# Kernel optimization log

Hardware: AMD Instinct MI355X
Metric: run time of the kernel (lower is better)

The kernel has to match this reference:

```python
import jax, jax.numpy as jnp
import numpy as np

B, S, H0G, H1G, H0E, H1E, A, E = 16384, 512, 512, 256, 1024, 512, 64, 4


def setup_inputs() -> dict:
    key = jax.random.key(0)
    ks = jax.random.split(key, 8)
    rn = lambda k, shape, s=0.05: jax.random.normal(k, shape, jnp.float32) * s
    return {
        "x": rn(ks[0], (B, S), 1.0),
        # Gating network params (Normalizer + 2 tanh layers + fca, softmax outside)
        "g_mean": jnp.zeros((S,), jnp.float32),
        "g_std": jnp.ones((S,), jnp.float32),
        "gW0": rn(ks[1], (S, H0G)), "gb0": jnp.zeros((H0G,), jnp.float32),
        "gW1": rn(ks[2], (H0G, H1G)), "gb1": jnp.zeros((H1G,), jnp.float32),
        "gWa": rn(ks[3], (H1G, E)), "gba": jnp.zeros((E,), jnp.float32),
        # 4 expert Actors, weights stacked along leading expert axis E
        "e_mean": jnp.zeros((E, S), jnp.float32),
        "e_std": jnp.ones((E, S), jnp.float32),
        "eW0": rn(ks[4], (E, S, H0E)), "eb0": jnp.zeros((E, H0E), jnp.float32),
        "eW1": rn(ks[5], (E, H0E, H1E)), "eb1": jnp.zeros((E, H1E), jnp.float32),
        "eWa": rn(ks[6], (E, H1E, A), 0.001), "eba": jnp.zeros((E, A), jnp.float32),
        "scale": jnp.ones((A,), jnp.float32),  # (a_max - a_min) / 2
    }


def reference(x, g_mean, g_std, gW0, gb0, gW1, gb1, gWa, gba,
              e_mean, e_std, eW0, eb0, eW1, eb1, eWa, eba, scale):
    # Gating: normalize -> tanh MLP -> linear -> softmax over experts
    xg = (x - g_mean) / g_std                                   # [B,S]
    h = jnp.tanh(xg @ gW0 + gb0)
    h = jnp.tanh(h @ gW1 + gb1)
    w = jax.nn.softmax(h @ gWa + gba, axis=-1)                  # [B,E]

    # Experts (Actor.forward), batched over expert axis e
    xe = (x[None, :, :] - e_mean[:, None, :]) / e_std[:, None, :]          # [E,B,S]
    he = jnp.tanh(jnp.einsum('ebs,esh->ebh', xe, eW0) + eb0[:, None, :])   # [E,B,H0E]
    he = jnp.tanh(jnp.einsum('ebh,ehk->ebk', he, eW1) + eb1[:, None, :])   # [E,B,H1E]
    a = (jnp.einsum('ebk,eka->eba', he, eWa) + eba[:, None, :]) * scale    # [E,B,A]

    # Weighted combination of expert action means
    return jnp.einsum('be,eba->ba', w, a)                       # [B,A]
```

## Files before the change

### kernel.cpp

```cpp
#include <hip/hip_runtime.h>
#include <hip/hip_bf16.h>

typedef _Float16 f16;
typedef _Float16 f16x4 __attribute__((ext_vector_type(4)));
typedef _Float16 f16x8 __attribute__((ext_vector_type(8)));
typedef float f32x4 __attribute__((ext_vector_type(4)));

#define DEV static __device__ __forceinline__

DEV void gld_lds16(const void* g, void* l) {
  __builtin_amdgcn_global_load_lds(
      (const __attribute__((address_space(1))) void*)g,
      (__attribute__((address_space(3))) void*)l, 16, 0, 0);
}

DEV float fast_tanh(float x) {
  float e = __expf(2.0f * x);
  return 1.0f - 2.0f / (e + 1.0f);
}

DEV int xcd_swizzle(int raw, int nwg) {
  return ((nwg & 7) == 0) ? ((raw & 7) * (nwg >> 3) + (raw >> 3)) : raw;
}

__global__ __launch_bounds__(256) void k_cvt_x(const float* __restrict__ x,
                                               f16* __restrict__ xh, long n) {
  long i0 = ((long)blockIdx.x * 256 + threadIdx.x) * 4;
  long stride = (long)gridDim.x * 1024;
  for (long i = i0; i < n; i += stride) {
    const float4 v = *(const float4*)(x + i);
    f16x4 h;
    h.x = (f16)v.x; h.y = (f16)v.y; h.z = (f16)v.z; h.w = (f16)v.w;
    *(f16x4*)(xh + i) = h;
  }
}

__global__ __launch_bounds__(256) void k_transpose(const float* __restrict__ in,
                                                   f16* __restrict__ out,
                                                   const float* __restrict__ stdv,
                                                   int K_, int N_) {
  __shared__ float tile[32][33];
  const int e = blockIdx.z;
  const float* ine = in + (long)e * K_ * N_;
  f16* oute = out + (long)e * K_ * N_;
  const int n0 = blockIdx.x * 32, k0 = blockIdx.y * 32;
  const int tx = threadIdx.x, ty = threadIdx.y;
#pragma unroll
  for (int j = 0; j < 4; j++)
    tile[ty + j * 8][tx] = ine[(long)(k0 + ty + j * 8) * N_ + n0 + tx];
  __syncthreads();
  const float rs = stdv ? 1.0f / stdv[(long)e * K_ + k0 + tx] : 1.0f;
#pragma unroll
  for (int j = 0; j < 4; j++)
    oute[(long)(n0 + ty + j * 8) * K_ + k0 + tx] = (f16)(tile[tx][ty + j * 8] * rs);
}

__global__ __launch_bounds__(1024) void k_bias_corr(const float* __restrict__ W,
                                                    const float* __restrict__ b,
                                                    const float* __restrict__ mean,
                                                    const float* __restrict__ stdv,
                                                    float* __restrict__ outb,
                                                    int S_, int H_) {
  __shared__ float red[16][64];
  const int e = blockIdx.y;
  const float* We = W + (long)e * S_ * H_;
  const float* me = mean + (long)e * S_;
  const float* se = stdv + (long)e * S_;
  const int h = blockIdx.x * 64 + threadIdx.x;
  const int sl = threadIdx.y;
  float acc = 0.0f;
#pragma unroll 4
  for (int s = sl; s < S_; s += 16) acc += (me[s] / se[s]) * We[(long)s * H_ + h];
  red[sl][threadIdx.x] = acc;
  __syncthreads();
  if (sl == 0) {
    float a = 0.0f;
#pragma unroll
    for (int j = 0; j < 16; j++) a += red[j][threadIdx.x];
    outb[(long)e * H_ + h] = b[(long)e * H_ + h] - a;
  }
}

__global__ __launch_bounds__(256) void k_gemm_cv(
    const f16* __restrict__ A, const f16* __restrict__ Bt,
    const float* __restrict__ bias, f16* __restrict__ C,
    int M, int K, int lda, int ldb, int ldc,
    long sA, long sB, long sBias, long sC) {
  A += (long)blockIdx.z * sA; Bt += (long)blockIdx.z * sB;
  bias += (long)blockIdx.z * sBias; C += (long)blockIdx.z * sC;
  extern __shared__ __align__(16) f16 lds[];
  const int tid = threadIdx.x, wave = tid >> 6, lane = tid & 63;
  const int nwg = gridDim.x * gridDim.y;
  const int logical = xcd_swizzle(blockIdx.y * gridDim.x + blockIdx.x, nwg);
  const int bx = logical % gridDim.x, by = logical / gridDim.x;
  const int m0 = by * 128, n0 = bx * 128;
  const int wr = wave >> 1, wc = wave & 1;
  f32x4 acc[4][4] = {};
  const int swz = (tid & 7) ^ ((tid >> 3) & 7);
  const f16* Ag = A + (long)(m0 + (tid >> 3)) * lda + swz * 8;
  const f16* Bg = Bt + (long)(n0 + (tid >> 3)) * ldb + swz * 8;
  const int wo = wave * 512;

#define STG_A(bufi, tile)                                         \
  { f16* _d = lds + (bufi) * 8192 + wo;                           \
    const long _k = (long)(tile) << 6;                            \
    gld_lds16(Ag + _k, _d);                                       \
    gld_lds16(Ag + (long)32 * lda + _k, _d + 2048);               \
    gld_lds16(Ag + (long)64 * lda + _k, _d + 4096);               \
    gld_lds16(Ag + (long)96 * lda + _k, _d + 6144); }
#define STG_B(bufi, tile)                                         \
  { f16* _d = lds + 24576 + (bufi) * 8192 + wo;                   \
    const long _k = (long)(tile) << 6;                            \
    gld_lds16(Bg + _k, _d);                                       \
    gld_lds16(Bg + (long)32 * ldb + _k, _d + 2048);               \
    gld_lds16(Bg + (long)64 * ldb + _k, _d + 4096);               \
    gld_lds16(Bg + (long)96 * ldb + _k, _d + 6144); }

  const int nt = K >> 6;
  STG_A(0, 0)
  STG_B(0, 0)
  STG_A(1, 1)
  asm volatile("s_waitcnt vmcnt(4)" ::: "memory");
  __builtin_amdgcn_s_barrier();
  asm volatile("" ::: "memory");

  for (int t = 0; t < nt; ++t) {
    if (t + 1 < nt) STG_B((t + 1) & 1, t + 1)
    if (t + 2 < nt) STG_A((t + 2) % 3, t + 2)
    const f16* Abuf = lds + (t % 3) * 8192;
    const f16* Bbuf = lds + 24576 + (t & 1) * 8192;
#pragma unroll
    for (int kk = 0; kk < 2; kk++) {
      f16x8 af[4], bfr[4];
      const int rchunk = (kk * 4 + (lane >> 4)) ^ (lane & 7);
#pragma unroll
      for (int mi = 0; mi < 4; mi++)
        af[mi] = *(const f16x8*)&Abuf[(wr * 64 + mi * 16 + (lane & 15)) * 64 + rchunk * 8];
#pragma unroll
      for (int ni = 0; ni < 4; ni++)
        bfr[ni] = *(const f16x8*)&Bbuf[(wc * 64 + ni * 16 + (lane & 15)) * 64 + rchunk * 8];
#pragma unroll
      for (int mi = 0; mi < 4; mi++)
#pragma unroll
        for (int ni = 0; ni < 4; ni++)
          acc[mi][ni] = __builtin_amdgcn_mfma_f32_16x16x32_f16(af[mi], bfr[ni], acc[mi][ni], 0, 0, 0);
    }
    if (t + 2 < nt) {
      asm volatile("s_waitcnt vmcnt(4)" ::: "memory");
    } else {
      asm volatile("s_waitcnt vmcnt(0)" ::: "memory");
    }
    __builtin_amdgcn_s_barrier();
    asm volatile("" ::: "memory");
  }
#undef STG_A
#undef STG_B

  const int r0 = (lane >> 4) * 4, cb = lane & 15;
#pragma unroll
  for (int ni = 0; ni < 4; ni++) {
    const int col = n0 + wc * 64 + ni * 16 + cb;
    const float bc = bias[col];
#pragma unroll
    for (int mi = 0; mi < 4; mi++) {
      const int row = m0 + wr * 64 + mi * 16 + r0;
#pragma unroll
      for (int r = 0; r < 4; r++)
        C[(long)(row + r) * ldc + col] = (f16)fast_tanh(acc[mi][ni][r] + bc);
    }
  }
}

__global__ __launch_bounds__(256) void k_gating_head(const f16* __restrict__ h1,
                                                     const float* __restrict__ gWa,
                                                     const float* __restrict__ gba,
                                                     float* __restrict__ gw, int B_) {
  const int b = blockIdx.x * 4 + (threadIdx.x >> 6);
  const int lane = threadIdx.x & 63;
  const f16x4 hv = *(const f16x4*)&h1[(long)b * 256 + lane * 4];
  float s0 = 0, s1 = 0, s2 = 0, s3 = 0;
#pragma unroll
  for (int j = 0; j < 4; j++) {
    const float hh = (float)hv[j];
    const float4 wr4 = *(const float4*)&gWa[(lane * 4 + j) * 4];
    s0 += hh * wr4.x; s1 += hh * wr4.y; s2 += hh * wr4.z; s3 += hh * wr4.w;
  }
#pragma unroll
  for (int off = 32; off >= 1; off >>= 1) {
    s0 += __shfl_xor(s0, off);
    s1 += __shfl_xor(s1, off);
    s2 += __shfl_xor(s2, off);
    s3 += __shfl_xor(s3, off);
  }
  const float l0 = s0 + gba[0], l1 = s1 + gba[1], l2 = s2 + gba[2], l3 = s3 + gba[3];
  float mx = fmaxf(fmaxf(l0, l1), fmaxf(l2, l3));
  const float e0 = __expf(l0 - mx), e1 = __expf(l1 - mx), e2 = __expf(l2 - mx), e3 = __expf(l3 - mx);
  const float inv = 1.0f / (e0 + e1 + e2 + e3);
  if (lane == 0) {
    float4 o; o.x = e0 * inv; o.y = e1 * inv; o.z = e2 * inv; o.w = e3 * inv;
    *(float4*)&gw[(long)b * 4] = o;
  }
}

__global__ __launch_bounds__(256) void k_head2(const f16* __restrict__ he1,
                                               const f16* __restrict__ Wt,
                                               const float* __restrict__ eba,
                                               const float* __restrict__ scale,
                                               const float* __restrict__ gw,
                                               float* __restrict__ out,
                                               long sA) {
  constexpr int K = 512;
  __shared__ __align__(16) f16 As[2][64 * 64];
  __shared__ __align__(16) f16 Bs[2][64 * 64];
  const int tid = threadIdx.x, wave = tid >> 6, lane = tid & 63;
  const int bid = xcd_swizzle(blockIdx.x, gridDim.x);
  const long m0 = (long)bid * 64;
  const int swz = (tid & 7) ^ ((tid >> 3) & 7);
  const f16* Ag = he1 + (m0 + tid / 8) * K + swz * 8;
  const f16* Bg = Wt + (long)(tid / 8) * K + swz * 8;
  const int wo = wave * 512;
  const int r0 = (lane >> 4) * 4, cb = lane & 15;
  float4 gwv[4];
#pragma unroll
  for (int r = 0; r < 4; r++)
    gwv[r] = *(const float4*)&gw[(m0 + wave * 16 + r0 + r) * 4];
  f32x4 osum[4] = {};
  f32x4 acc[4] = {};

#pragma unroll
  for (int i = 0; i < 2; i++) {
    gld_lds16(Ag + (long)i * 32 * K, &As[0][wo + i * 2048]);
    gld_lds16(Bg + (long)i * 32 * K, &Bs[0][wo + i * 2048]);
  }
  __syncthreads();
  int cur = 0;
#pragma unroll
  for (int e = 0; e < 4; e++) {
    for (int kt = 0; kt < 8; ++kt) {
      const int s = e * 8 + kt;
      if (s + 1 < 32) {
        const int sn = s + 1;
        const long ae = (long)(sn >> 3) * sA + ((sn & 7) << 6);
        const long be = (long)(sn >> 3) * (64 * K) + ((sn & 7) << 6);
#pragma unroll
        for (int i = 0; i < 2; i++) {
          gld_lds16(Ag + ae + (long)i * 32 * K, &As[cur ^ 1][wo + i * 2048]);
          gld_lds16(Bg + be + (long)i * 32 * K, &Bs[cur ^ 1][wo + i * 2048]);
        }
      }
#pragma unroll
      for (int kk = 0; kk < 2; kk++) {
        const int rchunk = (kk * 4 + (lane >> 4)) ^ (lane & 7);
        const f16x8 a = *(const f16x8*)&As[cur][(wave * 16 + (lane & 15)) * 64 + rchunk * 8];
#pragma unroll
        for (int ni = 0; ni < 4; ni++) {
          const f16x8 bq = *(const f16x8*)&Bs[cur][(ni * 16 + (lane & 15)) * 64 + rchunk * 8];
          acc[ni] = __builtin_amdgcn_mfma_f32_16x16x32_f16(a, bq, acc[ni], 0, 0, 0);
        }
      }
      __syncthreads();
      cur ^= 1;
    }
#pragma unroll
    for (int ni = 0; ni < 4; ni++)
#pragma unroll
      for (int r = 0; r < 4; r++) {
        const float ge = (e == 0) ? gwv[r].x : (e == 1) ? gwv[r].y
                        : (e == 2) ? gwv[r].z : gwv[r].w;
        osum[ni][r] += ge * acc[ni][r];
        acc[ni][r] = 0.0f;
      }
  }

#pragma unroll
  for (int ni = 0; ni < 4; ni++) {
    const int col = ni * 16 + cb;
    const float sc = scale[col];
#pragma unroll
    for (int r = 0; r < 4; r++) {
      const long row = m0 + wave * 16 + r0 + r;
      const float b4 = gwv[r].x * eba[col] + gwv[r].y * eba[64 + col] +
                       gwv[r].z * eba[128 + col] + gwv[r].w * eba[192 + col];
      out[row * 64 + col] = (osum[ni][r] + b4) * sc;
    }
  }
}

__global__ __launch_bounds__(256) void k_head(const f16* __restrict__ he1,
                                              const f16* __restrict__ Wt,
                                              const float* __restrict__ ebae,
                                              const float* __restrict__ scale,
                                              const float* __restrict__ gw,
                                              float* __restrict__ outa,
                                              int e0, int K,
                                              long sA, long sB, long sBias, long sC) {
  const int z = blockIdx.z;
  he1 += (long)z * sA; Wt += (long)z * sB; ebae += (long)z * sBias; outa += (long)z * sC;
  const int e = e0 + z;
  __shared__ __align__(16) f16 As[2][64 * 64];
  __shared__ __align__(16) f16 Bs[2][64 * 64];
  const int tid = threadIdx.x, wave = tid >> 6, lane = tid & 63;
  const int bid = xcd_swizzle(blockIdx.x, gridDim.x);
  const long m0 = (long)bid * 64;
  f32x4 acc[4] = {};
  const int swz = (tid & 7) ^ ((tid >> 3) & 7);
  const f16* Ag = he1 + (m0 + tid / 8) * K + swz * 8;
  const f16* Bg = Wt + (long)(tid / 8) * K + swz * 8;
  const int wo = wave * 512;
#pragma unroll
  for (int i = 0; i < 2; i++) {
    gld_lds16(Ag + (long)i * 32 * K, &As[0][wo + i * 2048]);
    gld_lds16(Bg + (long)i * 32 * K, &Bs[0][wo + i * 2048]);
  }
  __syncthreads();
  const int nt = K >> 6;
  int cur = 0;
  for (int t = 0; t < nt; ++t) {
    if (t + 1 < nt) {
      const long kt = (long)(t + 1) << 6;
#pragma unroll
      for (int i = 0; i < 2; i++) {
        gld_lds16(Ag + (long)i * 32 * K + kt, &As[cur ^ 1][wo + i * 2048]);
        gld_lds16(Bg + (long)i * 32 * K + kt, &Bs[cur ^ 1][wo + i * 2048]);
      }
    }
#pragma unroll
    for (int kk = 0; kk < 2; kk++) {
      const int rchunk = (kk * 4 + (lane >> 4)) ^ (lane & 7);
      const f16x8 a = *(const f16x8*)&As[cur][(wave * 16 + (lane & 15)) * 64 + rchunk * 8];
#pragma unroll
      for (int ni = 0; ni < 4; ni++) {
        const f16x8 bq = *(const f16x8*)&Bs[cur][(ni * 16 + (lane & 15)) * 64 + rchunk * 8];
        acc[ni] = __builtin_amdgcn_mfma_f32_16x16x32_f16(a, bq, acc[ni], 0, 0, 0);
      }
    }
    __syncthreads();
    cur ^= 1;
  }
  const int r0 = (lane >> 4) * 4, cb = lane & 15;
#pragma unroll
  for (int ni = 0; ni < 4; ni++) {
    const int col = ni * 16 + cb;
    const float sb = scale[col], bb = ebae[col];
    const long row0 = m0 + wave * 16 + r0;
#pragma unroll
    for (int r = 0; r < 4; r++) {
      const long row = row0 + r;
      outa[row * 64 + col] = (acc[ni][r] + bb) * sb * gw[row * 4 + e];
    }
  }
}

__global__ __launch_bounds__(256) void k_combine(const float* __restrict__ a_all,
                                                 float* __restrict__ out, long n) {
  long i = ((long)blockIdx.x * 256 + threadIdx.x) * 4;
  if (i < n) {
    const float4 v0 = *(const float4*)(a_all + i);
    const float4 v1 = *(const float4*)(a_all + n + i);
    const float4 v2 = *(const float4*)(a_all + 2 * n + i);
    const float4 v3 = *(const float4*)(a_all + 3 * n + i);
    float4 o;
    o.x = v0.x + v1.x + v2.x + v3.x;
    o.y = v0.y + v1.y + v2.y + v3.y;
    o.z = v0.z + v1.z + v2.z + v3.z;
    o.w = v0.w + v1.w + v2.w + v3.w;
    *(float4*)(out + i) = o;
  }
}

extern "C" void kernel_launch(void* const* d_in, const int* in_sizes, int n_in,
                              void* d_out, int out_size, void* d_ws, size_t ws_size,
                              hipStream_t stream) {
  constexpr int Bn = 16384, S = 512, H0G = 512, H1G = 256, H0E = 1024, H1E = 512, A = 64, E = 4;
  const float* x      = (const float*)d_in[0];
  const float* g_mean = (const float*)d_in[1];
  const float* g_std  = (const float*)d_in[2];
  const float* gW0    = (const float*)d_in[3];
  const float* gb0    = (const float*)d_in[4];
  const float* gW1    = (const float*)d_in[5];
  const float* gb1    = (const float*)d_in[6];
  const float* gWa    = (const float*)d_in[7];
  const float* gba    = (const float*)d_in[8];
  const float* e_mean = (const float*)d_in[9];
  const float* e_std  = (const float*)d_in[10];
  const float* eW0    = (const float*)d_in[11];
  const float* eb0    = (const float*)d_in[12];
  const float* eW1    = (const float*)d_in[13];
  const float* eb1    = (const float*)d_in[14];
  const float* eWa    = (const float*)d_in[15];
  const float* eba    = (const float*)d_in[16];
  const float* scale  = (const float*)d_in[17];
  float* out = (float*)d_out;

  char* p = (char*)d_ws;
  auto alloc = [&](size_t bytes) { char* q = p; p += (bytes + 255) & ~(size_t)255; return q; };
  f16* xh    = (f16*)alloc((size_t)Bn * S * 2);
  float* gw  = (float*)alloc((size_t)Bn * E * 4);
  float* a_all = (float*)alloc((size_t)E * Bn * A * 4);
  f16* gW0t  = (f16*)alloc((size_t)S * H0G * 2);
  f16* gW1t  = (f16*)alloc((size_t)H0G * H1G * 2);
  f16* eW0t  = (f16*)alloc((size_t)E * S * H0E * 2);
  f16* eW1t  = (f16*)alloc((size_t)E * H0E * H1E * 2);
  f16* eWat  = (f16*)alloc((size_t)E * H1E * A * 2);
  float* gb0c = (float*)alloc((size_t)H0G * 4);
  float* eb0c = (float*)alloc((size_t)E * H0E * 4);
  f16* h0g   = (f16*)alloc((size_t)Bn * H0G * 2);
  const size_t base = (size_t)(p - (char*)d_ws);
  const size_t per_g = ((size_t)Bn * H0E * 2 + 256) + ((size_t)Bn * H1E * 2 + 256);
  int g = 1;
  if (ws_size >= base + 4 * per_g) g = 4;
  else if (ws_size >= base + 2 * per_g) g = 2;
  f16* he0_g = (f16*)alloc((size_t)g * Bn * H0E * 2);
  f16* he1_g = (f16*)alloc((size_t)g * Bn * H1E * 2);
  f16* h1g = he1_g;

  k_cvt_x<<<2048, 256, 0, stream>>>(x, xh, (long)Bn * S);
  k_transpose<<<dim3(H0G / 32, S / 32, 1), dim3(32, 8), 0, stream>>>(gW0, gW0t, g_std, S, H0G);
  k_transpose<<<dim3(H1G / 32, H0G / 32, 1), dim3(32, 8), 0, stream>>>(gW1, gW1t, nullptr, H0G, H1G);
  k_transpose<<<dim3(H0E / 32, S / 32, E), dim3(32, 8), 0, stream>>>(eW0, eW0t, e_std, S, H0E);
  k_transpose<<<dim3(H1E / 32, H0E / 32, E), dim3(32, 8), 0, stream>>>(eW1, eW1t, nullptr, H0E, H1E);
  k_transpose<<<dim3(A / 32, H1E / 32, E), dim3(32, 8), 0, stream>>>(eWa, eWat, nullptr, H1E, A);
  k_bias_corr<<<dim3(H0G / 64, 1), dim3(64, 16), 0, stream>>>(gW0, gb0, g_mean, g_std, gb0c, S, H0G);
  k_bias_corr<<<dim3(H0E / 64, E), dim3(64, 16), 0, stream>>>(eW0, eb0, e_mean, e_std, eb0c, S, H0E);

  constexpr size_t LDSCV = 5 * 128 * 64 * sizeof(f16);

  k_gemm_cv<<<dim3(H0G / 128, Bn / 128, 1), 256, LDSCV, stream>>>(
      xh, gW0t, gb0c, h0g, Bn, S, S, S, H0G, 0, 0, 0, 0);
  k_gemm_cv<<<dim3(H1G / 128, Bn / 128, 1), 256, LDSCV, stream>>>(
      h0g, gW1t, gb1, h1g, Bn, H0G, H0G, H0G, H1G, 0, 0, 0, 0);
  k_gating_head<<<Bn / 4, 256, 0, stream>>>(h1g, gWa, gba, gw, Bn);

  if (g == 4) {
    k_gemm_cv<<<dim3(H0E / 128, Bn / 128, 4), 256, LDSCV, stream>>>(
        xh, eW0t, eb0c, he0_g, Bn, S, S, S, H0E,
        0, (long)S * H0E, H0E, (long)Bn * H0E);
    k_gemm_cv<<<dim3(H1E / 128, Bn / 128, 4), 256, LDSCV, stream>>>(
        he0_g, eW1t, eb1, he1_g, Bn, H0E, H0E, H0E, H1E,
        (long)Bn * H0E, (long)H0E * H1E, H1E, (long)Bn * H1E);
    k_head2<<<dim3(Bn / 64), 256, 0, stream>>>(
        he1_g, eWat, eba, scale, gw, out, (long)Bn * H1E);
  } else {
    for (int e0 = 0; e0 < E; e0 += g) {
      k_gemm_cv<<<dim3(H0E / 128, Bn / 128, g), 256, LDSCV, stream>>>(
          xh, eW0t + (size_t)e0 * S * H0E, eb0c + (size_t)e0 * H0E, he0_g,
          Bn, S, S, S, H0E,
          0, (long)S * H0E, H0E, (long)Bn * H0E);
      k_gemm_cv<<<dim3(H1E / 128, Bn / 128, g), 256, LDSCV, stream>>>(
          he0_g, eW1t + (size_t)e0 * H0E * H1E, eb1 + (size_t)e0 * H1E, he1_g,
          Bn, H0E, H0E, H0E, H1E,
          (long)Bn * H0E, (long)H0E * H1E, H1E, (long)Bn * H1E);
      k_head<<<dim3(Bn / 64, 1, g), 256, 0, stream>>>(
          he1_g, eWat + (size_t)e0 * H1E * A, eba + (size_t)e0 * A, scale, gw,
          a_all + (size_t)e0 * Bn * A, e0, H1E,
          (long)Bn * H1E, (long)H1E * A, A, (long)Bn * A);
    }
    k_combine<<<(Bn * A) / 1024, 256, 0, stream>>>(a_all, out, (long)Bn * A);
  }
}
```

Before: 296.7 us.

## Add 256x256-tile 8-wave GEMM with interleaved staging for expert layers

Measured after the change: 293.9 us (median of 2 runs). No clear change (-0.9%).

```diff
diff --git a/kernel.cpp b/kernel.cpp
--- a/kernel.cpp
+++ b/kernel.cpp
@@ -167,6 +167,121 @@
 #pragma unroll
       for (int r = 0; r < 4; r++)
         C[(long)(row + r) * ldc + col] = (f16)fast_tanh(acc[mi][ni][r] + bc);
+    }
+  }
+}
+
+__global__ __launch_bounds__(512, 2) void k_gemm_8p(
+    const f16* __restrict__ A, const f16* __restrict__ Bt,
+    const float* __restrict__ bias, f16* __restrict__ C,
+    int M, int K, int lda, int ldb, int ldc,
+    long sA, long sB, long sBias, long sC) {
+  A += (long)blockIdx.z * sA; Bt += (long)blockIdx.z * sB;
+  bias += (long)blockIdx.z * sBias; C += (long)blockIdx.z * sC;
+  extern __shared__ __align__(16) f16 lds[];
+  const int tid = threadIdx.x, wave = tid >> 6, lane = tid & 63;
+  const int nwg = gridDim.x * gridDim.y;
+  const int logical = xcd_swizzle(blockIdx.y * gridDim.x + blockIdx.x, nwg);
+  const int bx = logical % gridDim.x, by = logical / gridDim.x;
+  const int m0 = by * 256, n0 = bx * 256;
+  const int wr = wave >> 2, wc = wave & 3;
+  f32x4 acc[8][4] = {};
+
+  const int swz = (tid & 7) ^ ((tid >> 3) & 7);
+  const f16* Ag = A + (long)(m0 + (tid >> 3)) * lda + swz * 8;
+  const f16* Bg = Bt + (long)(n0 + (tid >> 3)) * ldb + swz * 8;
+  const int tdst = tid * 8;
+
+  const int rc0 = (lane >> 4) ^ (lane & 7);
+  const int rc1 = (4 + (lane >> 4)) ^ (lane & 7);
+  int aoff[8], boff[4];
+#pragma unroll
+  for (int mi = 0; mi < 8; mi++) aoff[mi] = (wr * 128 + mi * 16 + (lane & 15)) * 64;
+#pragma unroll
+  for (int ni = 0; ni < 4; ni++) boff[ni] = 16384 + (wc * 64 + ni * 16 + (lane & 15)) * 64;
+
+#define STG_A(jt, h)                                                          \
+  { f16* _d = lds + ((jt) & 1) * 32768 + (h) * 8192 + tdst;                   \
+    const long _k = (long)(jt) << 6;                                          \
+    gld_lds16(Ag + (long)((h) * 128) * lda + _k, _d);                         \
+    gld_lds16(Ag + (long)((h) * 128 + 64) * lda + _k, _d + 4096); }
+#define STG_B(jt, h)                                                          \
+  { f16* _d = lds + ((jt) & 1) * 32768 + 16384 + (h) * 8192 + tdst;           \
+    const long _k = (long)(jt) << 6;                                          \
+    gld_lds16(Bg + (long)((h) * 128) * ldb + _k, _d);                         \
+    gld_lds16(Bg + (long)((h) * 128 + 64) * ldb + _k, _d + 4096); }
+#define LOAD_A(b, rc)                                                         \
+  _Pragma("unroll") for (int mi = 0; mi < 8; mi++)                            \
+      af[mi] = *(const f16x8*)&lds[(b) * 32768 + aoff[mi] + (rc) * 8];
+#define LOAD_B(b, ni, rc)                                                     \
+  bfr[ni] = *(const f16x8*)&lds[(b) * 32768 + boff[ni] + (rc) * 8];
+#define MMA2(nA, nB)                                                          \
+  __builtin_amdgcn_s_setprio(1);                                              \
+  _Pragma("unroll") for (int mi = 0; mi < 8; mi++) {                          \
+    acc[mi][nA] = __builtin_amdgcn_mfma_f32_16x16x32_f16(af[mi], bfr[nA], acc[mi][nA], 0, 0, 0); \
+    acc[mi][nB] = __builtin_amdgcn_mfma_f32_16x16x32_f16(af[mi], bfr[nB], acc[mi][nB], 0, 0, 0); \
+  }                                                                           \
+  __builtin_amdgcn_s_setprio(0);
+#define BAR()                                                                 \
+  __builtin_amdgcn_s_barrier();                                               \
+  asm volatile("" ::: "memory")
+#define WAITL()                                                               \
+  asm volatile("s_waitcnt lgkmcnt(0)" ::: "memory");                          \
+  __builtin_amdgcn_sched_barrier(0)
+
+  const int nt = K >> 6;
+
+  STG_A(0, 0) STG_A(0, 1) STG_B(0, 0) STG_B(0, 1)
+  STG_A(1, 0)
+  asm volatile("s_waitcnt vmcnt(2)" ::: "memory");
+  BAR();
+
+  f16x8 af[8], bfr[4];
+  for (int j = 0; j < nt; ++j) {
+    const int b = j & 1;
+    LOAD_A(b, rc0) LOAD_B(b, 0, rc0) LOAD_B(b, 1, rc0)
+    if (j + 1 < nt) STG_A(j + 1, 1)
+    BAR(); WAITL(); MMA2(0, 1) BAR();
+    LOAD_B(b, 2, rc0) LOAD_B(b, 3, rc0)
+    if (j + 1 < nt) STG_B(j + 1, 0)
+    BAR(); WAITL(); MMA2(2, 3) BAR();
+    LOAD_A(b, rc1) LOAD_B(b, 0, rc1) LOAD_B(b, 1, rc1)
+    if (j + 1 < nt) STG_B(j + 1, 1)
+    BAR(); WAITL(); MMA2(0, 1) BAR();
+    LOAD_B(b, 2, rc1) LOAD_B(b, 3, rc1)
+    if (j + 2 < nt) STG_A(j + 2, 0)
+    BAR(); WAITL(); MMA2(2, 3)
+    if (j + 1 < nt) {
+      if (j + 2 < nt) {
+        asm volatile("s_waitcnt vmcnt(2)" ::: "memory");
+      } else {
+        asm volatile("s_waitcnt vmcnt(0)" ::: "memory");
+      }
+    }
+    BAR();
+  }
+#undef STG_A
+#undef STG_B
+#undef LOAD_A
+#undef LOAD_B
+#undef MMA2
+#undef BAR
+#undef WAITL
+
+  const int r0 = (lane >> 4) * 4, cb = lane & 15;
+  float bcv[4];
+#pragma unroll
+  for (int ni = 0; ni < 4; ni++) bcv[ni] = bias[n0 + wc * 64 + ni * 16 + cb];
+#pragma unroll
+  for (int mi = 0; mi < 8; mi++) {
+#pragma unroll
+    for (int r = 0; r < 4; r++) {
+      const long row = m0 + wr * 128 + mi * 16 + r0 + r;
+#pragma unroll
+      for (int ni = 0; ni < 4; ni++) {
+        const int col = n0 + wc * 64 + ni * 16 + cb;
+        C[row * (long)ldc + col] = (f16)fast_tanh(acc[mi][ni][r] + bcv[ni]);
+      }
     }
   }
 }
@@ -424,6 +539,7 @@
   k_bias_corr<<<dim3(H0E / 64, E), dim3(64, 16), 0, stream>>>(eW0, eb0, e_mean, e_std, eb0c, S, H0E);
 
   constexpr size_t LDSCV = 5 * 128 * 64 * sizeof(f16);
+  constexpr size_t LDS8P = 2 * 2 * 256 * 64 * sizeof(f16);
 
   k_gemm_cv<<<dim3(H0G / 128, Bn / 128, 1), 256, LDSCV, stream>>>(
       xh, gW0t, gb0c, h0g, Bn, S, S, S, H0G, 0, 0, 0, 0);
@@ -432,10 +548,10 @@
   k_gating_head<<<Bn / 4, 256, 0, stream>>>(h1g, gWa, gba, gw, Bn);
 
   if (g == 4) {
-    k_gemm_cv<<<dim3(H0E / 128, Bn / 128, 4), 256, LDSCV, stream>>>(
+    k_gemm_8p<<<dim3(H0E / 256, Bn / 256, 4), 512, LDS8P, stream>>>(
         xh, eW0t, eb0c, he0_g, Bn, S, S, S, H0E,
         0, (long)S * H0E, H0E, (long)Bn * H0E);
-    k_gemm_cv<<<dim3(H1E / 128, Bn / 128, 4), 256, LDSCV, stream>>>(
+    k_gemm_8p<<<dim3(H1E / 256, Bn / 256, 4), 512, LDS8P, stream>>>(
         he0_g, eW1t, eb1, he1_g, Bn, H0E, H0E, H0E, H1E,
         (long)Bn * H0E, (long)H0E * H1E, H1E, (long)Bn * H1E);
     k_head2<<<dim3(Bn / 64), 256, 0, stream>>>(
```
